# Performance work log

Measured on AMD Instinct MI355X. Metric: run time of the kernel, lower is better.

The kernel has to match this reference:

```python
import jax, jax.numpy as jnp
import numpy as np

B, T, C, H = 2, 2048, 1024, 16
D = C // H  # head dim = 64


def setup_inputs() -> dict:
    key = jax.random.key(0)
    k1, k2, k3 = jax.random.split(key, 3)
    s = 1.0 / np.sqrt(C)
    return {
        "x": jax.random.normal(k1, (B, T, C), dtype=jnp.float32),
        "w_qkv": jax.random.normal(k2, (C, 3 * C), dtype=jnp.float32) * s,
        "b_qkv": jnp.zeros((3 * C,), dtype=jnp.float32),
        "w_proj": jax.random.normal(k3, (C, C), dtype=jnp.float32) * s,
        "b_proj": jnp.zeros((C,), dtype=jnp.float32),
    }


def reference(x, w_qkv, b_qkv, w_proj, b_proj):
    Bx, Tx, Cx = x.shape
    qkv = x @ w_qkv + b_qkv                      # [B,T,3C]
    q, k, v = jnp.split(qkv, 3, axis=-1)         # each [B,T,C]
    # split heads -> [B,H,T,D]
    q = q.reshape(Bx, Tx, H, D).transpose(0, 2, 1, 3)
    k = k.reshape(Bx, Tx, H, D).transpose(0, 2, 1, 3)
    v = v.reshape(Bx, Tx, H, D).transpose(0, 2, 1, 3)
    att = jnp.einsum("bhqd,bhkd->bhqk", q, k) * (1.0 / np.sqrt(D))
    causal = jnp.tril(jnp.ones((Tx, Tx), dtype=bool))
    att = jnp.where(causal, att, -jnp.inf)
    att = jax.nn.softmax(att, axis=-1)
    y = jnp.einsum("bhqk,bhkd->bhqd", att, v)    # [B,H,T,D]
    y = y.transpose(0, 2, 1, 3).reshape(Bx, Tx, Cx)
    return y @ w_proj + b_proj
```

## Files before the change

kernel.cpp:

```cpp
#include <hip/hip_runtime.h>


typedef __attribute__((ext_vector_type(8))) __bf16 bf16x8;
typedef __attribute__((ext_vector_type(4))) float f32x4;
typedef __attribute__((ext_vector_type(8))) unsigned short u16x8;
typedef __attribute__((ext_vector_type(4))) unsigned short u16x4;

#define GAS __attribute__((address_space(1)))
#define LAS __attribute__((address_space(3)))

__device__ __forceinline__ unsigned short f2b(float f) {
  unsigned int u = __float_as_uint(f);
  unsigned int r = 0x7FFFu + ((u >> 16) & 1u);
  return (unsigned short)((u + r) >> 16);
}


__global__ void cvt_f32_to_bf16(const float* __restrict__ src,
                                unsigned short* __restrict__ dst, int n4) {
  int i = blockIdx.x * blockDim.x + threadIdx.x;
  if (i < n4) {
    float4 v = ((const float4*)src)[i];
    u16x4 o = { f2b(v.x), f2b(v.y), f2b(v.z), f2b(v.w) };
    *(u16x4*)(dst + (size_t)i * 4) = o;
  }
}

__global__ void transpose_f32_to_bf16(const float* __restrict__ src,
                                      unsigned short* __restrict__ dst,
                                      int K, int N) {
  __shared__ float tile[32][33];
  int n0 = blockIdx.x * 32, k0 = blockIdx.y * 32;
  int tx = threadIdx.x, ty = threadIdx.y;
#pragma unroll
  for (int i = 0; i < 32; i += 8)
    tile[ty + i][tx] = src[(size_t)(k0 + ty + i) * N + n0 + tx];
  __syncthreads();
#pragma unroll
  for (int i = 0; i < 32; i += 8)
    dst[(size_t)(n0 + ty + i) * K + k0 + tx] = f2b(tile[tx][ty + i]);
}


template <int MODE>
__global__ void __launch_bounds__(256) gemm_bt(
    const unsigned short* __restrict__ A, const unsigned short* __restrict__ Bt,
    const float* __restrict__ bias,
    unsigned short* __restrict__ Oq, unsigned short* __restrict__ Ok,
    unsigned short* __restrict__ Ov, float* __restrict__ Of,
    int M, int N, int K) {
  __shared__ unsigned short smem[4 * 128 * 64];
  unsigned short* As = smem;
  unsigned short* Bs = smem + 2 * 128 * 64;

  const int tid = threadIdx.x;
  const int lane = tid & 63;
  const int wid = tid >> 6;
  const int wr = wid >> 1, wc = wid & 1;
  const int lr = lane & 15, lg = lane >> 4;
  const int m0 = blockIdx.x * 128;
  const int n0 = blockIdx.y * 128;

  f32x4 acc[4][4];
#pragma unroll
  for (int mi = 0; mi < 4; mi++)
#pragma unroll
    for (int ni = 0; ni < 4; ni++) acc[mi][ni] = (f32x4){0.f, 0.f, 0.f, 0.f};

  auto stage = [&](int t, int buf) {
    const int k0 = t * 64;
    unsigned short* Ad = As + buf * (128 * 64);
    unsigned short* Bd = Bs + buf * (128 * 64);
#pragma unroll
    for (int it = 0; it < 4; ++it) {
      const int chunk_u = it * 256 + (tid & ~63);
      const int chunk = chunk_u + lane;
      const int row = chunk >> 3;
      const int col = ((chunk & 7) ^ (row & 7)) * 8;
      __builtin_amdgcn_global_load_lds(
          (GAS unsigned int*)(A + (size_t)(m0 + row) * K + k0 + col),
          (LAS unsigned int*)(Ad + chunk_u * 8), 16, 0, 0);
      __builtin_amdgcn_global_load_lds(
          (GAS unsigned int*)(Bt + (size_t)(n0 + row) * K + k0 + col),
          (LAS unsigned int*)(Bd + chunk_u * 8), 16, 0, 0);
    }
  };

  const int swa = (lr & 7) * 8;
  const int kt = K >> 6;

  stage(0, 0);

  for (int t = 0; t < kt; ++t) {
    const int cur = t & 1;
    __builtin_amdgcn_s_barrier();
    if (t + 1 < kt) {
      stage(t + 1, cur ^ 1);
      asm volatile("s_waitcnt vmcnt(8)" ::: "memory");
    } else {
      asm volatile("s_waitcnt vmcnt(0)" ::: "memory");
    }
    __builtin_amdgcn_s_barrier();

    const unsigned short* Ab = As + cur * (128 * 64);
    const unsigned short* Bb = Bs + cur * (128 * 64);

#pragma unroll
    for (int kk = 0; kk < 2; ++kk) {
      bf16x8 af[4], bfr[4];
#pragma unroll
      for (int mi = 0; mi < 4; mi++)
        af[mi] = *(const bf16x8*)(Ab + (wr * 64 + mi * 16 + lr) * 64 +
                                  ((kk * 32 + lg * 8) ^ swa));
#pragma unroll
      for (int ni = 0; ni < 4; ni++)
        bfr[ni] = *(const bf16x8*)(Bb + (wc * 64 + ni * 16 + lr) * 64 +
                                   ((kk * 32 + lg * 8) ^ swa));
#pragma unroll
      for (int mi = 0; mi < 4; mi++)
#pragma unroll
        for (int ni = 0; ni < 4; ni++)
          acc[mi][ni] = __builtin_amdgcn_mfma_f32_16x16x32_bf16(
              af[mi], bfr[ni], acc[mi][ni], 0, 0, 0);
    }
  }

  const float SCLQ = 0.125f * 1.44269504088896340736f;

  if constexpr (MODE == 1) {
#pragma unroll
    for (int mi = 0; mi < 4; mi++) {
#pragma unroll
      for (int ni = 0; ni < 4; ni++) {
        const int nn = n0 + wc * 64 + ni * 16 + lr;
        const float bv = bias[nn];
#pragma unroll
        for (int r = 0; r < 4; r++) {
          const int mm = m0 + wr * 64 + mi * 16 + lg * 4 + r;
          Of[(size_t)mm * N + nn] = acc[mi][ni][r] + bv;
        }
      }
    }
  } else {
    unsigned short* L = smem;
    const int which = n0 >> 10;
    const float sc = (which == 0) ? SCLQ : 1.0f;
    __syncthreads();
#pragma unroll
    for (int mi = 0; mi < 4; mi++) {
#pragma unroll
      for (int ni = 0; ni < 4; ni++) {
        const int nn_l = wc * 64 + ni * 16 + lr;
        const float bv = bias[n0 + nn_l];
#pragma unroll
        for (int r = 0; r < 4; r++) {
          const int mm_l = wr * 64 + mi * 16 + lg * 4 + r;
          const unsigned short v = f2b((acc[mi][ni][r] + bv) * sc);
          if (which == 2) L[nn_l * 136 + mm_l] = v;
          else            L[mm_l * 136 + nn_l] = v;
        }
      }
    }
    __syncthreads();
    const int b = m0 >> 11;
    const int t0 = m0 & 2047;
    const int h0 = (n0 & 1023) >> 6;
    if (which == 2) {
      const int row = tid >> 1;
      const int hsub = row >> 6, d = row & 63;
      const int tt0 = (tid & 1) * 64;
      const unsigned short* src = L + row * 136 + tt0;
      unsigned short* dst = Ov +
          ((size_t)((b * 16 + h0 + hsub) * 64 + d)) * 2048 + t0 + tt0;
#pragma unroll
      for (int j = 0; j < 8; j++)
        *(u16x8*)(dst + j * 8) = *(const u16x8*)(src + j * 8);
    } else {
      const int mm_l = tid & 127;
      const int hsub = tid >> 7;
      const unsigned short* src = L + mm_l * 136 + hsub * 64;
      unsigned short* base = (which == 0) ? Oq : Ok;
      unsigned short* dst = base +
          ((size_t)(b * 16 + h0 + hsub) * 2048 + t0 + mm_l) * 64;
#pragma unroll
      for (int j = 0; j < 8; j++)
        *(u16x8*)(dst + j * 8) = *(const u16x8*)(src + j * 8);
    }
  }
}


__global__ void __launch_bounds__(512) attn_kernel(
    const unsigned short* __restrict__ Qh, const unsigned short* __restrict__ Kh,
    const unsigned short* __restrict__ Vh, unsigned short* __restrict__ yatt) {
  __shared__ unsigned short KsL[2 * 64 * 64];
  __shared__ unsigned short VsL[2 * 64 * 64];
  __shared__ unsigned short Pl[8 * 16 * 72];

  const int tid = threadIdx.x;
  const int lane = tid & 63;
  const int w = tid >> 6;
  const int lr = lane & 15, lg = lane >> 4;

  const int bh = blockIdx.x & 31;
  const int qt = 15 - (blockIdx.x >> 5);
  const int hh = bh & 15;
  const int bb = bh >> 4;
  const int ntiles = 2 * qt + 2;
  const int diagw = 2 * qt + ((w >> 2) & 1);

  const size_t head_base = ((size_t)(bb * 16 + hh)) * 2048 * 64;
  const unsigned short* Qg = Qh + head_base;
  const unsigned short* Kg = Kh + head_base;
  const unsigned short* Vg = Vh + head_base;

  const int q0 = qt * 128 + w * 16;

  bf16x8 aq0 = *(const bf16x8*)(Qg + (size_t)(q0 + lr) * 64 + lg * 8);
  bf16x8 aq1 = *(const bf16x8*)(Qg + (size_t)(q0 + lr) * 64 + 32 + lg * 8);

  bf16x8 vones;
#pragma unroll
  for (int j = 0; j < 8; j++) vones[j] = (__bf16)1.0f;

  float m_run[4], l_run[4];
  f32x4 acc_o[4];
#pragma unroll
  for (int r = 0; r < 4; r++) { m_run[r] = -__builtin_inff(); l_run[r] = 0.f; }
#pragma unroll
  for (int dj = 0; dj < 4; dj++) acc_o[dj] = (f32x4){0.f, 0.f, 0.f, 0.f};

  const int srow = tid >> 3;
  const int scol = (((tid & 7) ^ (srow & 7)) << 3);

  auto stage = [&](int kv0, int buf) {
    unsigned short* Kd = KsL + buf * (64 * 64);
    unsigned short* Vd = VsL + buf * (64 * 64);
    const int base_u = (tid & ~63) * 8;
    __builtin_amdgcn_global_load_lds(
        (GAS unsigned int*)(Kg + (size_t)(kv0 + srow) * 64 + scol),
        (LAS unsigned int*)(Kd + base_u), 16, 0, 0);
    __builtin_amdgcn_global_load_lds(
        (GAS unsigned int*)(Vg + (size_t)srow * 2048 + kv0 + scol),
        (LAS unsigned int*)(Vd + base_u), 16, 0, 0);
  };

  __bf16* Pw = (__bf16*)(Pl + w * 16 * 72);
  const int swr = (lr & 7) << 3;

  stage(0, 0);

  for (int i = 0; i < ntiles; ++i) {
    const int cur = i & 1;
    __builtin_amdgcn_s_barrier();
    if (i + 1 < ntiles) {
      stage((i + 1) * 64, cur ^ 1);
      asm volatile("s_waitcnt vmcnt(2)" ::: "memory");
    } else {
      asm volatile("s_waitcnt vmcnt(0)" ::: "memory");
    }
    __builtin_amdgcn_s_barrier();

    if (i <= diagw) {
      const int kv0 = i * 64;
      const unsigned short* Kb = KsL + cur * (64 * 64);
      const unsigned short* Vb = VsL + cur * (64 * 64);

      f32x4 s[4];
#pragma unroll
      for (int nj = 0; nj < 4; nj++) {
        const unsigned short* krow = Kb + (nj * 16 + lr) * 64;
        bf16x8 kb0 = *(const bf16x8*)(krow + ((lg * 8) ^ swr));
        bf16x8 kb1 = *(const bf16x8*)(krow + ((32 + lg * 8) ^ swr));
        f32x4 z = (f32x4){0.f, 0.f, 0.f, 0.f};
        z = __builtin_amdgcn_mfma_f32_16x16x32_bf16(aq0, kb0, z, 0, 0, 0);
        z = __builtin_amdgcn_mfma_f32_16x16x32_bf16(aq1, kb1, z, 0, 0, 0);
        s[nj] = z;
      }

      if (i == diagw) {
#pragma unroll
        for (int nj = 0; nj < 4; nj++) {
          const int key = kv0 + nj * 16 + lr;
#pragma unroll
          for (int r = 0; r < 4; r++) {
            const int qrow = q0 + lg * 4 + r;
            if (key > qrow) s[nj][r] = -__builtin_inff();
          }
        }
      }

      float pm[4];
#pragma unroll
      for (int r = 0; r < 4; r++)
        pm[r] = fmaxf(fmaxf(s[0][r], s[1][r]), fmaxf(s[2][r], s[3][r]));

      const bool okl = (pm[0] <= m_run[0] + 8.f) & (pm[1] <= m_run[1] + 8.f) &
                       (pm[2] <= m_run[2] + 8.f) & (pm[3] <= m_run[3] + 8.f);
      if (!__all(okl)) {
#pragma unroll
        for (int r = 0; r < 4; r++) {
#pragma unroll
          for (int off = 1; off < 16; off <<= 1)
            pm[r] = fmaxf(pm[r], __shfl_xor(pm[r], off));
          const float mn = fmaxf(m_run[r], pm[r]);
          const float sc = exp2f(m_run[r] - mn);
          m_run[r] = mn;
          l_run[r] *= sc;
#pragma unroll
          for (int dj = 0; dj < 4; dj++) acc_o[dj][r] *= sc;
        }
      }

#pragma unroll
      for (int nj = 0; nj < 4; nj++) {
#pragma unroll
        for (int r = 0; r < 4; r++) {
          const float p = exp2f(s[nj][r] - m_run[r]);
          Pw[(lg * 4 + r) * 72 + nj * 16 + lr] = (__bf16)p;
        }
      }

      bf16x8 pa0 = *(const bf16x8*)(Pw + lr * 72 + lg * 8);
      bf16x8 pa1 = *(const bf16x8*)(Pw + lr * 72 + 32 + lg * 8);

      f32x4 zs = (f32x4){0.f, 0.f, 0.f, 0.f};
      zs = __builtin_amdgcn_mfma_f32_16x16x32_bf16(pa0, vones, zs, 0, 0, 0);
      zs = __builtin_amdgcn_mfma_f32_16x16x32_bf16(pa1, vones, zs, 0, 0, 0);

#pragma unroll
      for (int dj = 0; dj < 4; dj++) {
        const unsigned short* vrow = Vb + (dj * 16 + lr) * 64;
        bf16x8 vb0 = *(const bf16x8*)(vrow + ((lg * 8) ^ swr));
        bf16x8 vb1 = *(const bf16x8*)(vrow + ((32 + lg * 8) ^ swr));
        acc_o[dj] = __builtin_amdgcn_mfma_f32_16x16x32_bf16(pa0, vb0, acc_o[dj], 0, 0, 0);
        acc_o[dj] = __builtin_amdgcn_mfma_f32_16x16x32_bf16(pa1, vb1, acc_o[dj], 0, 0, 0);
      }

#pragma unroll
      for (int r = 0; r < 4; r++) l_run[r] += zs[r];
    }
  }

  __bf16* yb = (__bf16*)yatt;
#pragma unroll
  for (int r = 0; r < 4; r++) {
    const float inv = 1.0f / l_run[r];
    const int t = q0 + lg * 4 + r;
    const size_t rowbase = ((size_t)(bb * 2048 + t)) * 1024 + hh * 64;
#pragma unroll
    for (int dj = 0; dj < 4; dj++)
      yb[rowbase + dj * 16 + lr] = (__bf16)(acc_o[dj][r] * inv);
  }
}


extern "C" void kernel_launch(void* const* d_in, const int* in_sizes, int n_in,
                              void* d_out, int out_size, void* d_ws,
                              size_t ws_size, hipStream_t stream) {
  (void)in_sizes; (void)n_in; (void)out_size; (void)ws_size;
  const float* x      = (const float*)d_in[0];
  const float* w_qkv  = (const float*)d_in[1];
  const float* b_qkv  = (const float*)d_in[2];
  const float* w_proj = (const float*)d_in[3];
  const float* b_proj = (const float*)d_in[4];
  float* out = (float*)d_out;

  unsigned short* ws     = (unsigned short*)d_ws;
  unsigned short* xb     = ws;
  unsigned short* wqkvT  = xb     + (size_t)4096 * 1024;
  unsigned short* wprojT = wqkvT  + (size_t)3072 * 1024;
  unsigned short* Qh     = wprojT + (size_t)1024 * 1024;
  unsigned short* Kh     = Qh     + (size_t)2 * 16 * 2048 * 64;
  unsigned short* Vh     = Kh     + (size_t)2 * 16 * 2048 * 64;
  unsigned short* yatt   = Vh     + (size_t)2 * 16 * 2048 * 64;

  cvt_f32_to_bf16<<<4096, 256, 0, stream>>>(x, xb, 1048576);
  transpose_f32_to_bf16<<<dim3(96, 32), dim3(32, 8), 0, stream>>>(w_qkv, wqkvT, 1024, 3072);
  transpose_f32_to_bf16<<<dim3(32, 32), dim3(32, 8), 0, stream>>>(w_proj, wprojT, 1024, 1024);

  gemm_bt<0><<<dim3(32, 24), 256, 0, stream>>>(xb, wqkvT, b_qkv, Qh, Kh, Vh,
                                               nullptr, 4096, 3072, 1024);
  attn_kernel<<<512, 512, 0, stream>>>(Qh, Kh, Vh, yatt);
  gemm_bt<1><<<dim3(32, 8), 256, 0, stream>>>(yatt, wprojT, b_proj, nullptr,
                                              nullptr, nullptr, out, 4096, 1024, 1024);
}
```

Baseline: 124.3 us.

## Split long causal attention rows across two blocks and merge partial softmax results

The attention grid grows from 512 to 896 blocks. For the later query tiles (qt 4-15), the KV range is split into two halves computed by separate blocks, which write unnormalized bf16 partial outputs together with running max and sum to workspace. A new merge kernel combines the halves with log-sum-exp weighting. This is meant to balance the causal triangle's uneven work and fill more CUs. It costs an extra launch, extra workspace traffic, and bf16 rounding of the partials. The partials reuse the xb workspace region, which is dead after the QKV GEMM. s_setprio hints are also added around the MFMA sections in the GEMM and attention kernels.

Measured after the change: 121.2 us. 2.6% less time.

```diff
diff --git a/kernel.cpp b/kernel.cpp
--- a/kernel.cpp
+++ b/kernel.cpp
@@ -13,6 +13,9 @@
   unsigned int u = __float_as_uint(f);
   unsigned int r = 0x7FFFu + ((u >> 16) & 1u);
   return (unsigned short)((u + r) >> 16);
+}
+__device__ __forceinline__ float b2f(unsigned short u) {
+  return __uint_as_float((unsigned int)u << 16);
 }
 
 
@@ -116,12 +119,14 @@
       for (int ni = 0; ni < 4; ni++)
         bfr[ni] = *(const bf16x8*)(Bb + (wc * 64 + ni * 16 + lr) * 64 +
                                    ((kk * 32 + lg * 8) ^ swa));
+      __builtin_amdgcn_s_setprio(1);
 #pragma unroll
       for (int mi = 0; mi < 4; mi++)
 #pragma unroll
         for (int ni = 0; ni < 4; ni++)
           acc[mi][ni] = __builtin_amdgcn_mfma_f32_16x16x32_bf16(
               af[mi], bfr[ni], acc[mi][ni], 0, 0, 0);
+      __builtin_amdgcn_s_setprio(0);
     }
   }
 
@@ -192,7 +197,9 @@
 
 __global__ void __launch_bounds__(512) attn_kernel(
     const unsigned short* __restrict__ Qh, const unsigned short* __restrict__ Kh,
-    const unsigned short* __restrict__ Vh, unsigned short* __restrict__ yatt) {
+    const unsigned short* __restrict__ Vh, unsigned short* __restrict__ yatt,
+    unsigned short* __restrict__ Opart, float* __restrict__ Mp,
+    float* __restrict__ Lp) {
   __shared__ unsigned short KsL[2 * 64 * 64];
   __shared__ unsigned short VsL[2 * 64 * 64];
   __shared__ unsigned short Pl[8 * 16 * 72];
@@ -202,12 +209,19 @@
   const int w = tid >> 6;
   const int lr = lane & 15, lg = lane >> 4;
 
+  const int cls = blockIdx.x >> 5;
   const int bh = blockIdx.x & 31;
-  const int qt = 15 - (blockIdx.x >> 5);
   const int hh = bh & 15;
   const int bb = bh >> 4;
-  const int ntiles = 2 * qt + 2;
-  const int diagw = 2 * qt + ((w >> 2) & 1);
+
+  const unsigned long long QA = 0x8899AABBCCDDEEFFull;
+  const unsigned long long QB = 0x0000014425566377ull;
+  const unsigned long long KK = 0x00A4912444444444ull;
+  const int qt = (cls < 16) ? (int)((QA >> (4 * cls)) & 15)
+                            : (int)((QB >> (4 * (cls - 16))) & 15);
+  const int kind = (int)((KK >> (2 * cls)) & 3);
+  const int t0 = (kind == 1) ? (qt + 1) : 0;
+  const int t1 = (kind == 0) ? (qt + 1) : (2 * qt + 2);
 
   const size_t head_base = ((size_t)(bb * 16 + hh)) * 2048 * 64;
   const unsigned short* Qg = Qh + head_base;
@@ -215,6 +229,7 @@
   const unsigned short* Vg = Vh + head_base;
 
   const int q0 = qt * 128 + w * 16;
+  const int diagw = 2 * qt + ((w >> 2) & 1);
 
   bf16x8 aq0 = *(const bf16x8*)(Qg + (size_t)(q0 + lr) * 64 + lg * 8);
   bf16x8 aq1 = *(const bf16x8*)(Qg + (size_t)(q0 + lr) * 64 + 32 + lg * 8);
@@ -248,12 +263,12 @@
   __bf16* Pw = (__bf16*)(Pl + w * 16 * 72);
   const int swr = (lr & 7) << 3;
 
-  stage(0, 0);
-
-  for (int i = 0; i < ntiles; ++i) {
+  stage(t0 * 64, t0 & 1);
+
+  for (int i = t0; i < t1; ++i) {
     const int cur = i & 1;
     __builtin_amdgcn_s_barrier();
-    if (i + 1 < ntiles) {
+    if (i + 1 < t1) {
       stage((i + 1) * 64, cur ^ 1);
       asm volatile("s_waitcnt vmcnt(2)" ::: "memory");
     } else {
@@ -267,6 +282,7 @@
       const unsigned short* Vb = VsL + cur * (64 * 64);
 
       f32x4 s[4];
+      __builtin_amdgcn_s_setprio(1);
 #pragma unroll
       for (int nj = 0; nj < 4; nj++) {
         const unsigned short* krow = Kb + (nj * 16 + lr) * 64;
@@ -277,6 +293,7 @@
         z = __builtin_amdgcn_mfma_f32_16x16x32_bf16(aq1, kb1, z, 0, 0, 0);
         s[nj] = z;
       }
+      __builtin_amdgcn_s_setprio(0);
 
       if (i == diagw) {
 #pragma unroll
@@ -324,6 +341,7 @@
       bf16x8 pa0 = *(const bf16x8*)(Pw + lr * 72 + lg * 8);
       bf16x8 pa1 = *(const bf16x8*)(Pw + lr * 72 + 32 + lg * 8);
 
+      __builtin_amdgcn_s_setprio(1);
       f32x4 zs = (f32x4){0.f, 0.f, 0.f, 0.f};
       zs = __builtin_amdgcn_mfma_f32_16x16x32_bf16(pa0, vones, zs, 0, 0, 0);
       zs = __builtin_amdgcn_mfma_f32_16x16x32_bf16(pa1, vones, zs, 0, 0, 0);
@@ -336,22 +354,64 @@
         acc_o[dj] = __builtin_amdgcn_mfma_f32_16x16x32_bf16(pa0, vb0, acc_o[dj], 0, 0, 0);
         acc_o[dj] = __builtin_amdgcn_mfma_f32_16x16x32_bf16(pa1, vb1, acc_o[dj], 0, 0, 0);
       }
+      __builtin_amdgcn_s_setprio(0);
 
 #pragma unroll
       for (int r = 0; r < 4; r++) l_run[r] += zs[r];
     }
   }
 
-  __bf16* yb = (__bf16*)yatt;
-#pragma unroll
-  for (int r = 0; r < 4; r++) {
-    const float inv = 1.0f / l_run[r];
-    const int t = q0 + lg * 4 + r;
-    const size_t rowbase = ((size_t)(bb * 2048 + t)) * 1024 + hh * 64;
-#pragma unroll
-    for (int dj = 0; dj < 4; dj++)
-      yb[rowbase + dj * 16 + lr] = (__bf16)(acc_o[dj][r] * inv);
+  if (kind == 2) {
+    __bf16* yb = (__bf16*)yatt;
+#pragma unroll
+    for (int r = 0; r < 4; r++) {
+      const float inv = 1.0f / l_run[r];
+      const int t = q0 + lg * 4 + r;
+      const size_t rowbase = ((size_t)(bb * 2048 + t)) * 1024 + hh * 64;
+#pragma unroll
+      for (int dj = 0; dj < 4; dj++)
+        yb[rowbase + dj * 16 + lr] = (__bf16)(acc_o[dj][r] * inv);
+    }
+  } else {
+    __bf16* Ob = (__bf16*)Opart;
+#pragma unroll
+    for (int r = 0; r < 4; r++) {
+      const int slot = bh * 1536 + (q0 + lg * 4 + r) - 512;
+      const size_t obase = ((size_t)(kind * 49152 + slot)) * 64;
+#pragma unroll
+      for (int dj = 0; dj < 4; dj++)
+        Ob[obase + dj * 16 + lr] = (__bf16)acc_o[dj][r];
+      if (lr == 0) {
+        Mp[kind * 49152 + slot] = m_run[r];
+        Lp[kind * 49152 + slot] = l_run[r];
+      }
+    }
   }
+}
+
+__global__ void __launch_bounds__(256) attn_merge(
+    const unsigned short* __restrict__ Op, const float* __restrict__ Mp,
+    const float* __restrict__ Lp, unsigned short* __restrict__ yatt) {
+  const int gid = blockIdx.x * 256 + threadIdx.x;
+  const int sl = gid >> 3;
+  const int d0 = (gid & 7) * 8;
+  const int bh = blockIdx.y;
+  const int slot = bh * 1536 + sl;
+  const float m1 = Mp[slot], m2 = Mp[49152 + slot];
+  const float l1 = Lp[slot], l2 = Lp[49152 + slot];
+  const float mx = fmaxf(m1, m2);
+  const float w1 = exp2f(m1 - mx), w2 = exp2f(m2 - mx);
+  const float inv = 1.0f / (l1 * w1 + l2 * w2);
+  u16x8 a = *(const u16x8*)(Op + (size_t)slot * 64 + d0);
+  u16x8 b = *(const u16x8*)(Op + (size_t)(49152 + slot) * 64 + d0);
+  const int qr = 512 + sl;
+  unsigned short* dst = yatt +
+      ((size_t)((bh >> 4) * 2048 + qr)) * 1024 + (bh & 15) * 64 + d0;
+  u16x8 o;
+#pragma unroll
+  for (int j = 0; j < 8; j++)
+    o[j] = f2b((b2f(a[j]) * w1 + b2f(b[j]) * w2) * inv);
+  *(u16x8*)dst = o;
 }
 
 
@@ -375,13 +435,18 @@
   unsigned short* Vh     = Kh     + (size_t)2 * 16 * 2048 * 64;
   unsigned short* yatt   = Vh     + (size_t)2 * 16 * 2048 * 64;
 
+  unsigned short* Opart = ws;
+  float* Mp = (float*)(ws + (size_t)6291456);
+  float* Lp = Mp + 2 * 49152;
+
   cvt_f32_to_bf16<<<4096, 256, 0, stream>>>(x, xb, 1048576);
   transpose_f32_to_bf16<<<dim3(96, 32), dim3(32, 8), 0, stream>>>(w_qkv, wqkvT, 1024, 3072);
   transpose_f32_to_bf16<<<dim3(32, 32), dim3(32, 8), 0, stream>>>(w_proj, wprojT, 1024, 1024);
 
   gemm_bt<0><<<dim3(32, 24), 256, 0, stream>>>(xb, wqkvT, b_qkv, Qh, Kh, Vh,
                                                nullptr, 4096, 3072, 1024);
-  attn_kernel<<<512, 512, 0, stream>>>(Qh, Kh, Vh, yatt);
+  attn_kernel<<<896, 512, 0, stream>>>(Qh, Kh, Vh, yatt, Opart, Mp, Lp);
+  attn_merge<<<dim3(48, 32), 256, 0, stream>>>(Opart, Mp, Lp, yatt);
   gemm_bt<1><<<dim3(32, 8), 256, 0, stream>>>(yatt, wprojT, b_proj, nullptr,
                                               nullptr, nullptr, out, 4096, 1024, 1024);
 }
```
